# Optimization experiments

Measured on AMD Instinct MI355X. Metric: run time of the kernel, lower is better.

## Reference

```python
import jax, jax.numpy as jnp
import numpy as np

B, M, F1, F2, FILTERS = 64, 128, 32, 32, 32

def setup_inputs() -> dict:
    key = jax.random.key(0)
    k1, k2, k3, k4, k5 = jax.random.split(key, 5)
    sf1 = jax.random.normal(k1, (B, M, M, F1), dtype=jnp.float32)
    sf2 = jax.random.normal(k2, (B, M, M, F2), dtype=jnp.float32)
    # binary adjacency mask (sparse-ish neighbor structure), kept float as in the torch code
    adjacency = (jax.random.uniform(k3, (B, M, M)) < 0.1).astype(jnp.float32)
    W = jax.random.normal(k4, (F1 + F2, FILTERS), dtype=jnp.float32) * (1.414 * (6.0 / (F1 + F2 + FILTERS)) ** 0.5)
    b = jax.random.normal(k5, (1, FILTERS), dtype=jnp.float32) * 0.1
    return {"scalar_features_1": sf1, "scalar_features_2": sf2, "adjacency": adjacency, "W": W, "b": b}

def reference(scalar_features_1, scalar_features_2, adjacency, W, b):
    # concat pair features: [B, M, M, F1+F2]
    x = jnp.concatenate([scalar_features_1, scalar_features_2], axis=-1)
    # linear transform: [B, M, M, FILTERS]
    h = jnp.einsum('bijk,kf->bijf', x, W) + b
    # adjacency-masked sum pooling over the neighbor axis (axis=2)
    h = h * adjacency[..., None]
    return jnp.sum(h, axis=2)  # [B, M, FILTERS]
```

## Files before the change

kernel.cpp:

```cpp
#include <hip/hip_runtime.h>

#define B_DIM   64
#define M_DIM   128
#define F_HALF  32
#define K_DIM   64
#define NFILT   32

__global__ __launch_bounds__(256)
void gconv_kernel(const float* __restrict__ sf1,
                  const float* __restrict__ sf2,
                  const float* __restrict__ adj,
                  const float* __restrict__ W,
                  const float* __restrict__ bias,
                  float* __restrict__ out)
{
    __shared__ float s_adj[M_DIM];
    __shared__ int   s_idx[M_DIM];
    __shared__ int   s_cnt;
    __shared__ float s_deg;
    __shared__ float s_acc[4][K_DIM];
    __shared__ float s_y[K_DIM];
    __shared__ float s_W[K_DIM * NFILT];

    const int bid  = blockIdx.x;
    const int t    = threadIdx.x;
    const int w    = t >> 6;
    const int lane = t & 63;

    if (t == 0) s_cnt = 0;

    #pragma unroll
    for (int r = 0; r < 8; ++r)
        s_W[r * 256 + t] = W[r * 256 + t];

    __syncthreads();

    const float* adj_row = adj + (size_t)bid * M_DIM;
    if (t < M_DIM) {
        float a = adj_row[t];
        s_adj[t] = a;
        if (a != 0.0f) {
            int p = atomicAdd(&s_cnt, 1);
            s_idx[p] = t;
        }
    }
    __syncthreads();
    const int cnt = s_cnt;

    const size_t row_base = (size_t)bid * M_DIM * F_HALF;
    const float* base = (lane < F_HALF)
                          ? (sf1 + row_base + lane)
                          : (sf2 + row_base + (lane - F_HALF));

    float acc = 0.0f;
    for (int e = w; e < cnt; e += 16) {
        float a0 = 0.f, a1 = 0.f, a2 = 0.f, a3 = 0.f;
        float v0 = 0.f, v1 = 0.f, v2 = 0.f, v3 = 0.f;
        {
            int j = s_idx[e];
            a0 = s_adj[j];
            v0 = base[(size_t)j * F_HALF];
        }
        if (e + 4 < cnt) {
            int j = s_idx[e + 4];
            a1 = s_adj[j];
            v1 = base[(size_t)j * F_HALF];
        }
        if (e + 8 < cnt) {
            int j = s_idx[e + 8];
            a2 = s_adj[j];
            v2 = base[(size_t)j * F_HALF];
        }
        if (e + 12 < cnt) {
            int j = s_idx[e + 12];
            a3 = s_adj[j];
            v3 = base[(size_t)j * F_HALF];
        }
        acc += a0 * v0;
        acc += a1 * v1;
        acc += a2 * v2;
        acc += a3 * v3;
    }
    s_acc[w][lane] = acc;

    if (w == 1) {
        float d = s_adj[lane] + s_adj[lane + 64];
        #pragma unroll
        for (int off = 32; off; off >>= 1)
            d += __shfl_down(d, off);
        if (lane == 0) s_deg = d;
    }
    __syncthreads();

    if (t < K_DIM)
        s_y[t] = s_acc[0][t] + s_acc[1][t] + s_acc[2][t] + s_acc[3][t];
    __syncthreads();

    if (t < NFILT) {
        float o = s_deg * bias[t];
        #pragma unroll
        for (int k = 0; k < K_DIM; ++k)
            o += s_y[k] * s_W[k * NFILT + t];
        out[(size_t)bid * NFILT + t] = o;
    }
}

extern "C" void kernel_launch(void* const* d_in, const int* in_sizes, int n_in,
                              void* d_out, int out_size, void* d_ws, size_t ws_size,
                              hipStream_t stream) {
    const float* sf1  = (const float*)d_in[0];
    const float* sf2  = (const float*)d_in[1];
    const float* adj  = (const float*)d_in[2];
    const float* W    = (const float*)d_in[3];
    const float* bias = (const float*)d_in[4];
    float* out = (float*)d_out;

    gconv_kernel<<<B_DIM * M_DIM, 256, 0, stream>>>(sf1, sf2, adj, W, bias, out);
}
```

Before: 230.8 us.

## Map one adjacency row per wavefront using ballot masks instead of shared-memory compaction

Each 64-lane wavefront now handles one output row, so a block covers four rows. Nonzero neighbours are found with ballot bitmasks and ctz iteration, replacing the shared-memory atomic compaction and the block-wide barriers. The degree and the 64x32 projection are done with shuffles and W is read straight from global memory, which drops the shared-memory W staging. The price is one wave walking all neighbours serially with less memory-level parallelism per row, and no explicit unrolling of the gather loads.

```diff
diff --git a/kernel.cpp b/kernel.cpp
--- a/kernel.cpp
+++ b/kernel.cpp
@@ -7,102 +7,61 @@
 #define NFILT   32
 
 __global__ __launch_bounds__(256)
-void gconv_kernel(const float* __restrict__ sf1,
-                  const float* __restrict__ sf2,
-                  const float* __restrict__ adj,
-                  const float* __restrict__ W,
-                  const float* __restrict__ bias,
-                  float* __restrict__ out)
+void gconv_wave(const float* __restrict__ sf1,
+                const float* __restrict__ sf2,
+                const float* __restrict__ adj,
+                const float* __restrict__ W,
+                const float* __restrict__ bias,
+                float* __restrict__ out)
 {
-    __shared__ float s_adj[M_DIM];
-    __shared__ int   s_idx[M_DIM];
-    __shared__ int   s_cnt;
-    __shared__ float s_deg;
-    __shared__ float s_acc[4][K_DIM];
-    __shared__ float s_y[K_DIM];
-    __shared__ float s_W[K_DIM * NFILT];
+    const int t    = threadIdx.x;
+    const int lane = t & 63;
+    const int row  = blockIdx.x * 4 + (t >> 6);
 
-    const int bid  = blockIdx.x;
-    const int t    = threadIdx.x;
-    const int w    = t >> 6;
-    const int lane = t & 63;
+    const float* arow = adj + (size_t)row * M_DIM;
+    const float a_lo = arow[lane];
+    const float a_hi = arow[lane + 64];
 
-    if (t == 0) s_cnt = 0;
+    unsigned long long m0 = __ballot(a_lo != 0.0f);
+    unsigned long long m1 = __ballot(a_hi != 0.0f);
 
-    #pragma unroll
-    for (int r = 0; r < 8; ++r)
-        s_W[r * 256 + t] = W[r * 256 + t];
+    const size_t rb = (size_t)row * (M_DIM * F_HALF);
+    const float* base = (lane < F_HALF)
+                          ? (sf1 + rb + lane)
+                          : (sf2 + rb + (lane - F_HALF));
 
-    __syncthreads();
-
-    const float* adj_row = adj + (size_t)bid * M_DIM;
-    if (t < M_DIM) {
-        float a = adj_row[t];
-        s_adj[t] = a;
-        if (a != 0.0f) {
-            int p = atomicAdd(&s_cnt, 1);
-            s_idx[p] = t;
+    float acc = 0.0f;
+    float deg = 0.0f;
+    while (m0 | m1) {
+        if (m0) {
+            const int j = __builtin_ctzll(m0);
+            m0 &= (m0 - 1);
+            const float a = __shfl(a_lo, j);
+            const float v = base[(size_t)j * F_HALF];
+            acc += a * v;
+            deg += a;
+        }
+        if (m1) {
+            const int j = __builtin_ctzll(m1);
+            m1 &= (m1 - 1);
+            const float a = __shfl(a_hi, j);
+            const float v = base[(size_t)(j + 64) * F_HALF];
+            acc += a * v;
+            deg += a;
         }
     }
-    __syncthreads();
-    const int cnt = s_cnt;
 
-    const size_t row_base = (size_t)bid * M_DIM * F_HALF;
-    const float* base = (lane < F_HALF)
-                          ? (sf1 + row_base + lane)
-                          : (sf2 + row_base + (lane - F_HALF));
-
-    float acc = 0.0f;
-    for (int e = w; e < cnt; e += 16) {
-        float a0 = 0.f, a1 = 0.f, a2 = 0.f, a3 = 0.f;
-        float v0 = 0.f, v1 = 0.f, v2 = 0.f, v3 = 0.f;
-        {
-            int j = s_idx[e];
-            a0 = s_adj[j];
-            v0 = base[(size_t)j * F_HALF];
-        }
-        if (e + 4 < cnt) {
-            int j = s_idx[e + 4];
-            a1 = s_adj[j];
-            v1 = base[(size_t)j * F_HALF];
-        }
-        if (e + 8 < cnt) {
-            int j = s_idx[e + 8];
-            a2 = s_adj[j];
-            v2 = base[(size_t)j * F_HALF];
-        }
-        if (e + 12 < cnt) {
-            int j = s_idx[e + 12];
-            a3 = s_adj[j];
-            v3 = base[(size_t)j * F_HALF];
-        }
-        acc += a0 * v0;
-        acc += a1 * v1;
-        acc += a2 * v2;
-        acc += a3 * v3;
+    const int f     = lane & 31;
+    const int kbase = (lane >> 5) * 32;
+    float p = 0.0f;
+    #pragma unroll
+    for (int kk = 0; kk < 32; ++kk) {
+        const float yk = __shfl(acc, kbase + kk);
+        p += yk * W[(kbase + kk) * NFILT + f];
     }
-    s_acc[w][lane] = acc;
-
-    if (w == 1) {
-        float d = s_adj[lane] + s_adj[lane + 64];
-        #pragma unroll
-        for (int off = 32; off; off >>= 1)
-            d += __shfl_down(d, off);
-        if (lane == 0) s_deg = d;
-    }
-    __syncthreads();
-
-    if (t < K_DIM)
-        s_y[t] = s_acc[0][t] + s_acc[1][t] + s_acc[2][t] + s_acc[3][t];
-    __syncthreads();
-
-    if (t < NFILT) {
-        float o = s_deg * bias[t];
-        #pragma unroll
-        for (int k = 0; k < K_DIM; ++k)
-            o += s_y[k] * s_W[k * NFILT + t];
-        out[(size_t)bid * NFILT + t] = o;
-    }
+    p += __shfl_down(p, 32);
+    if (lane < 32)
+        out[(size_t)row * NFILT + f] = p + deg * bias[f];
 }
 
 extern "C" void kernel_launch(void* const* d_in, const int* in_sizes, int n_in,
@@ -115,5 +74,5 @@
     const float* bias = (const float*)d_in[4];
     float* out = (float*)d_out;
 
-    gconv_kernel<<<B_DIM * M_DIM, 256, 0, stream>>>(sf1, sf2, adj, W, bias, out);
+    gconv_wave<<<(B_DIM * M_DIM) / 4, 256, 0, stream>>>(sf1, sf2, adj, W, bias, out);
 }
```

Measured after the change: 232.1 us. No clear change (+0.6%).
